# Kernel optimization log

Hardware: AMD Instinct MI355X
Metric: run time of the kernel (lower is better)

Reference implementation:

```python
import jax, jax.numpy as jnp
import numpy as np

H = 8       # n_heads
E = 128     # embedding_size (= per-head dim)
NEG = -1000000000.0


def setup_inputs() -> dict:
    key = jax.random.key(0)
    ks = jax.random.split(key, 12)
    b, n = 8, 1024
    x = jax.random.normal(ks[0], (b, n, E), dtype=jnp.float32)
    dist = jax.random.normal(ks[1], (b, n, n), dtype=jnp.float32)
    mask = jax.random.randint(ks[2], (b, n), 0, 2).astype(jnp.float32)
    s = 1.0 / np.sqrt(E)
    Wq = jax.random.normal(ks[3], (E, H * E), dtype=jnp.float32) * s
    Wk = jax.random.normal(ks[4], (E, H * E), dtype=jnp.float32) * s
    Wv = jax.random.normal(ks[5], (E, H * E), dtype=jnp.float32) * s
    bq = jnp.zeros((H * E,), jnp.float32)
    bk = jnp.zeros((H * E,), jnp.float32)
    bv = jnp.zeros((H * E,), jnp.float32)
    Wo = jax.random.normal(ks[6], (H * E, E), dtype=jnp.float32) * (1.0 / np.sqrt(H * E))
    bo = jnp.zeros((E,), jnp.float32)
    return {"x": x, "dist": dist, "mask": mask, "Wq": Wq, "bq": bq,
            "Wk": Wk, "bk": bk, "Wv": Wv, "bv": bv, "Wo": Wo, "bo": bo}


def reference(x, dist, mask, Wq, bq, Wk, bk, Wv, bv, Wo, bo):
    b, n, e = x.shape
    scale = e ** (-0.5)
    # project and split heads: [b, n, H*E] -> [b, H, n, E]
    def heads(W, bias):
        return (x @ W + bias).reshape(b, n, H, e).transpose(0, 2, 1, 3)
    q = heads(Wq, bq) * mask[:, None, :, None]
    k = heads(Wk, bk) * mask[:, None, :, None]
    v = heads(Wv, bv) * mask[:, None, :, None]
    # scores with additive distance bias broadcast over heads
    a = jnp.einsum('bhqe,bhke->bhqk', q * scale, k) + dist[:, None, :, :]
    am = jnp.einsum('bq,bk->bqk', mask, mask)[:, None, :, :]  # [b,1,n,n]
    a = jnp.where(am == 0, NEG, a)
    a = jax.nn.softmax(a, axis=-1)
    a = jnp.where(am == 0, 0.0, a)
    y = jnp.einsum('bhqk,bhke->bhqe', a, v)
    y = y.transpose(0, 2, 1, 3).reshape(b, n, H * e)
    y = y @ Wo + bo
    return y * mask[:, :, None]
```

## Files before the change

kernel.cpp:

```cpp
#include <hip/hip_runtime.h>
#include <hip/hip_bf16.h>
#include <hip/hip_fp16.h>

#define NH 8
#define ED 128
#define NB 8
#define NN 1024

typedef __attribute__((ext_vector_type(8))) short s16x8;
typedef __attribute__((ext_vector_type(8))) __bf16 bf16x8_t;
typedef __attribute__((ext_vector_type(4))) float f32x4;
typedef __attribute__((ext_vector_type(16))) float f32x16;
typedef __attribute__((ext_vector_type(4))) unsigned int u32x4;

#define LOG2E 1.4426950408889634f
#define SINIT -23.083120654223414f

static __device__ __forceinline__ unsigned short f2bf(float f) {
    union { float f; unsigned u; } v; v.f = f;
    unsigned r = v.u + 0x7fffu + ((v.u >> 16) & 1u);
    return (unsigned short)(r >> 16);
}

static __device__ __forceinline__ f32x4 mfma16(s16x8 a, s16x8 b, f32x4 c) {
    return __builtin_amdgcn_mfma_f32_16x16x32_bf16(
        __builtin_bit_cast(bf16x8_t, a), __builtin_bit_cast(bf16x8_t, b), c, 0, 0, 0);
}

static __device__ __forceinline__ f32x16 mfma32(s16x8 a, s16x8 b, f32x16 c) {
    return __builtin_amdgcn_mfma_f32_32x32x16_bf16(
        __builtin_bit_cast(bf16x8_t, a), __builtin_bit_cast(bf16x8_t, b), c, 0, 0, 0);
}

static __device__ __forceinline__ unsigned cvtpk(float lo, float hi) {
    unsigned r;
    asm("v_cvt_pk_bf16_f32 %0, %1, %2" : "=v"(r) : "v"(lo), "v"(hi));
    return r;
}

static __device__ __forceinline__ void gll16(const void* g, void* l) {
    __builtin_amdgcn_global_load_lds((const __attribute__((address_space(1))) void*)g,
                                     (__attribute__((address_space(3))) void*)l, 16, 0, 0);
}

__global__ __launch_bounds__(256) void prep_xw_kernel(
    const float* __restrict__ x,
    const float* __restrict__ Wq, const float* __restrict__ Wk,
    const float* __restrict__ Wv, const float* __restrict__ Wo,
    unsigned short* __restrict__ xb,
    unsigned short* __restrict__ wqt, unsigned short* __restrict__ wkt,
    unsigned short* __restrict__ wvt, unsigned short* __restrict__ wot) {
    int bid = blockIdx.x, tid = threadIdx.x;
    if (bid < 1024) {
        int i = bid * 256 + tid;
        float4 v = ((const float4*)x)[i];
        unsigned long long pk = (unsigned long long)f2bf(v.x)
                              | ((unsigned long long)f2bf(v.y) << 16)
                              | ((unsigned long long)f2bf(v.z) << 32)
                              | ((unsigned long long)f2bf(v.w) << 48);
        ((unsigned long long*)xb)[i] = pk;
        return;
    }
    __shared__ __align__(16) float wtile[32][36];
    int wi = bid - 1024;
    int mat = wi >> 7, ti = wi & 127;
    const float* in; unsigned short* outp; int rows_in, cols_in, tr0, tc0;
    if (mat == 0)      { in = Wq; outp = wqt; rows_in = 128;  cols_in = 1024; }
    else if (mat == 1) { in = Wk; outp = wkt; rows_in = 128;  cols_in = 1024; }
    else if (mat == 2) { in = Wv; outp = wvt; rows_in = 128;  cols_in = 1024; }
    else               { in = Wo; outp = wot; rows_in = 1024; cols_in = 128;  }
    if (mat < 3) { tr0 = (ti >> 5) * 32; tc0 = (ti & 31) * 32; }
    else         { tr0 = (ti >> 2) * 32; tc0 = (ti & 3)  * 32; }

    {
        int r = tid >> 3, cs = tid & 7;
        f32x4 v = *(const f32x4*)(in + (size_t)(tr0 + r) * cols_in + tc0 + cs * 4);
        *(f32x4*)&wtile[r][cs * 4] = v;
    }
    __syncthreads();
    {
        int c = tid >> 3, rs = tid & 7;
        unsigned long long pk = (unsigned long long)f2bf(wtile[rs * 4 + 0][c])
                              | ((unsigned long long)f2bf(wtile[rs * 4 + 1][c]) << 16)
                              | ((unsigned long long)f2bf(wtile[rs * 4 + 2][c]) << 32)
                              | ((unsigned long long)f2bf(wtile[rs * 4 + 3][c]) << 48);
        *(unsigned long long*)(outp + (size_t)(tc0 + c) * rows_in + tr0 + rs * 4) = pk;
    }
}

__global__ __launch_bounds__(256) void qkv_dist_kernel(
    const unsigned short* __restrict__ xb,
    const unsigned short* __restrict__ wqt,
    const unsigned short* __restrict__ wkt,
    const unsigned short* __restrict__ wvt,
    const float* __restrict__ bq, const float* __restrict__ bk, const float* __restrict__ bv,
    const float* __restrict__ dist,
    const float* __restrict__ mask,
    unsigned short* __restrict__ q_ws,
    unsigned short* __restrict__ k_ws,
    unsigned short* __restrict__ v_ws,
    unsigned short* __restrict__ dswz) {
    int bid = blockIdx.x, tid = threadIdx.x;

    __shared__ __align__(16) unsigned short dt16[128][68];

    if (bid < 1024) {
        int kt = bid & 15;
        int t = bid >> 4;
        int qt = t & 7;
        int b = t >> 3;

        int seg = tid & 15, r0 = tid >> 4;
        const float* src = dist + ((size_t)b * NN + qt * 128) * NN + kt * 64;
        f32x4 m4 = *(const f32x4*)(mask + b * NN + kt * 64 + seg * 4);
#pragma unroll
        for (int pass = 0; pass < 8; ++pass) {
            int row = pass * 16 + r0;
            f32x4 d4 = *(const f32x4*)(src + (size_t)row * NN + seg * 4);
            unsigned long long pk = 0;
#pragma unroll
            for (int j = 0; j < 4; ++j) {
                unsigned short o = (m4[j] == 0.0f) ? (unsigned short)0xFBFF
                                 : __half_as_ushort(__float2half_rn(d4[j] * LOG2E));
                pk |= (unsigned long long)o << (16 * j);
            }
            *(unsigned long long*)&dt16[row][seg * 4] = pk;
        }
        __syncthreads();

        int h = (tid >> 5) & 1;
        int row = (tid >> 6) * 32 + (tid & 31);
#pragma unroll
        for (int c = 0; c < 4; ++c) {
            int colbase = (c >> 1) * 32 + (c & 1) * 16 + 4 * h;
            const unsigned short* rp = &dt16[row][0];
            u32x4 pk;
            pk[0] = *(const unsigned*)&rp[colbase];
            pk[1] = *(const unsigned*)&rp[colbase + 2];
            pk[2] = *(const unsigned*)&rp[colbase + 8];
            pk[3] = *(const unsigned*)&rp[colbase + 10];
            *(u32x4*)(dswz + ((size_t)(bid * 4 + c) * 256 + tid) * 8) = pk;
        }
        return;
    }

    int qb_ = bid - 1024;
    int mt = qb_ / 24, c = qb_ % 24;
    int which = c >> 3;
    int c0 = (c & 7) * 128;
    int m0 = mt * 128;
    int w = tid >> 6, lane = tid & 63, g = lane >> 4, r15 = lane & 15;
    int wr = (w >> 1) * 64, wc = (w & 1) * 64;

    const unsigned short* wt = (which == 0) ? wqt : (which == 1) ? wkt : wvt;
    const float* bias = (which == 0) ? bq : (which == 1) ? bk : bv;

    const f32x4 fzero = {0.f, 0.f, 0.f, 0.f};
    f32x4 acc[4][4];
#pragma unroll
    for (int i = 0; i < 4; i++)
#pragma unroll
        for (int j = 0; j < 4; j++) acc[i][j] = fzero;

#pragma unroll
    for (int kf = 0; kf < 4; kf++) {
        s16x8 af[4], bfr[4];
#pragma unroll
        for (int mf = 0; mf < 4; mf++)
            af[mf] = *(const s16x8*)(xb + (size_t)(m0 + wr + mf * 16 + r15) * ED + kf * 32 + g * 8);
#pragma unroll
        for (int nf = 0; nf < 4; nf++)
            bfr[nf] = *(const s16x8*)(wt + (size_t)(c0 + wc + nf * 16 + r15) * ED + kf * 32 + g * 8);
#pragma unroll
        for (int mf = 0; mf < 4; mf++)
#pragma unroll
            for (int nf = 0; nf < 4; nf++)
                acc[mf][nf] = mfma16(af[mf], bfr[nf], acc[mf][nf]);
    }

    float scale = (which == 0) ? 0.12751741566380696f : 1.0f;

#pragma unroll
    for (int nf = 0; nf < 4; nf++) {
        int col = c0 + wc + nf * 16 + r15;
        float bv_ = bias[col];
        int hh = col >> 7, e = col & 127;
#pragma unroll
        for (int mf = 0; mf < 4; mf++) {
#pragma unroll
            for (int rr = 0; rr < 4; rr++) {
                int row = m0 + wr + mf * 16 + g * 4 + rr;
                int bb = row >> 10, n = row & 1023;
                int bh = bb * NH + hh;
                float val = (acc[mf][nf][rr] + bv_) * scale;
                if (which == 0) {
                    q_ws[((size_t)bh * NN + n) * ED + e] = f2bf(val);
                } else if (which == 1) {
                    int ktl = n >> 6, k = n & 63;
                    int slot = (e >> 4) * 128 + ((e >> 3) & 1) * 64 + (k >> 5) * 32 + (k & 31);
                    k_ws[(size_t)(bh * 16 + ktl) * 8192 + slot * 8 + (e & 7)] = f2bf(val);
                } else {
                    int ktl = n >> 6, k = n & 63;
                    int slot = (k >> 4) * 256 + ((k >> 3) & 1) * 128 + (e >> 5) * 32 + (e & 31);
                    v_ws[(size_t)(bh * 16 + ktl) * 8192 + slot * 8 + (k & 7)] = f2bf(val);
                }
            }
        }
    }
}

__global__ __launch_bounds__(256) void attn_kernel(
    const unsigned short* __restrict__ q_ws,
    const unsigned short* __restrict__ k_ws,
    const unsigned short* __restrict__ v_ws,
    const unsigned short* __restrict__ dswz,
    unsigned short* __restrict__ y_ws) {
    int p = blockIdx.x;
    int b = p & 7, r = p >> 3;
    int head = r >> 3, qt = r & 7;
    int bh = b * NH + head;
    int q0 = qt * 128;

    int tid = threadIdx.x;
    int w = tid >> 6, lane = tid & 63;
    int e31 = lane & 31, h = lane >> 5;

    __shared__ __align__(16) unsigned short Kl[2][8192];
    __shared__ __align__(16) unsigned short Vl[2][8192];

    const char* kg = (const char*)k_ws + (size_t)bh * 16 * 16384;
    const char* vg = (const char*)v_ws + (size_t)bh * 16 * 16384;
    const char* dq = (const char*)dswz + ((size_t)(b * 8 + qt) << 18);

    int qrow = q0 + w * 32 + e31;
    s16x8 qf[8];
    const unsigned short* qb = q_ws + ((size_t)bh * NN + qrow) * ED + h * 8;
#pragma unroll
    for (int es = 0; es < 8; ++es) qf[es] = *(const s16x8*)(qb + es * 16);

    const f32x16 fz16 = {0.f,0.f,0.f,0.f,0.f,0.f,0.f,0.f,0.f,0.f,0.f,0.f,0.f,0.f,0.f,0.f};
    f32x16 sini;
#pragma unroll
    for (int i = 0; i < 16; ++i) sini[i] = SINIT;
    f32x16 o0 = fz16, o1 = fz16, o2 = fz16, o3 = fz16;
    float lacc[4] = {0.f, 0.f, 0.f, 0.f};

#pragma unroll
    for (int pass = 0; pass < 4; ++pass) {
        gll16(kg + (pass * 256 + tid) * 16, (char*)&Kl[0][0] + pass * 4096 + w * 1024);
        gll16(vg + (pass * 256 + tid) * 16, (char*)&Vl[0][0] + pass * 4096 + w * 1024);
    }
    __syncthreads();

    for (int kt = 0; kt < 16; ++kt) {
        int cur = kt & 1;
        if (kt < 15) {
            const char* kn = kg + (size_t)(kt + 1) * 16384;
            const char* vn = vg + (size_t)(kt + 1) * 16384;
            char* kd = (char*)&Kl[cur ^ 1][0] + w * 1024;
            char* vd = (char*)&Vl[cur ^ 1][0] + w * 1024;
#pragma unroll
            for (int pass = 0; pass < 4; ++pass) {
                gll16(kn + (pass * 256 + tid) * 16, kd + pass * 4096);
                gll16(vn + (pass * 256 + tid) * 16, vd + pass * 4096);
            }
        }

        u32x4 dch[4];
#pragma unroll
        for (int c = 0; c < 4; ++c)
            dch[c] = *(const u32x4*)(dq + ((size_t)(kt * 4 + c) * 256 + tid) * 16);

        const char* Kp = (const char*)&Kl[cur][0] + h * 1024 + e31 * 16;
        f32x16 sA0 = sini, sA1 = sini;
        __builtin_amdgcn_s_setprio(1);
#pragma unroll
        for (int es = 0; es < 8; ++es) {
            s16x8 kb0 = *(const s16x8*)(Kp + es * 2048);
            s16x8 kb1 = *(const s16x8*)(Kp + es * 2048 + 512);
            sA0 = mfma32(kb0, qf[es], sA0);
            sA1 = mfma32(kb1, qf[es], sA1);
        }
        __builtin_amdgcn_s_setprio(0);

        float pp[32];
#pragma unroll
        for (int c = 0; c < 4; ++c) {
            float lc = 0.f;
#pragma unroll
            for (int u = 0; u < 8; ++u) {
                int i = c * 8 + u;
                unsigned wv = dch[c][u >> 1];
                float dv = __half2float(__ushort_as_half(
                    (unsigned short)((u & 1) ? (wv >> 16) : (wv & 0xffff))));
                float sv = (i < 16) ? sA0[i] : sA1[i - 16];
                float pv = __builtin_exp2f(sv + dv);
                pp[i] = pv;
                lc += pv;
            }
            lacc[c] += lc;
        }

        const char* Vp = (const char*)&Vl[cur][0] + h * 2048 + e31 * 16;
        __builtin_amdgcn_s_setprio(1);
#pragma unroll
        for (int kf = 0; kf < 2; ++kf) {
#pragma unroll
            for (int ks2 = 0; ks2 < 2; ++ks2) {
                const float* pb = &pp[kf * 16 + ks2 * 8];
                unsigned A0 = cvtpk(pb[0], pb[1]);
                unsigned A1 = cvtpk(pb[2], pb[3]);
                unsigned B0 = cvtpk(pb[4], pb[5]);
                unsigned B1 = cvtpk(pb[6], pb[7]);
                asm("v_permlane32_swap_b32 %0, %1" : "+v"(A0), "+v"(B0));
                asm("v_permlane32_swap_b32 %0, %1" : "+v"(A1), "+v"(B1));
                u32x4 pw;
                pw[0] = A0;
                pw[1] = A1;
                pw[2] = B0;
                pw[3] = B1;
                s16x8 pa = __builtin_bit_cast(s16x8, pw);
                int kstep = kf * 2 + ks2;
                const char* vp = Vp + kstep * 4096;
                o0 = mfma32(pa, *(const s16x8*)(vp), o0);
                o1 = mfma32(pa, *(const s16x8*)(vp + 512), o1);
                o2 = mfma32(pa, *(const s16x8*)(vp + 1024), o2);
                o3 = mfma32(pa, *(const s16x8*)(vp + 1536), o3);
            }
        }
        __builtin_amdgcn_s_setprio(0);
        __syncthreads();
    }

    float l_r = (lacc[0] + lacc[1]) + (lacc[2] + lacc[3]);
    float lt = l_r + __shfl_xor(l_r, 32, 64);
    float inv = (lt > 0.f) ? 1.0f / lt : 0.f;
#pragma unroll
    for (int rc = 0; rc < 4; ++rc) {
#pragma unroll
        for (int jj = 0; jj < 4; ++jj) {
            int qq = jj + 8 * rc + 4 * h;
            float iq = __shfl(inv, qq, 64);
            int row = q0 + w * 32 + qq;
            size_t base = ((size_t)b * NN + row) * (NH * ED) + head * ED + e31;
            y_ws[base]      = f2bf(o0[rc * 4 + jj] * iq);
            y_ws[base + 32] = f2bf(o1[rc * 4 + jj] * iq);
            y_ws[base + 64] = f2bf(o2[rc * 4 + jj] * iq);
            y_ws[base + 96] = f2bf(o3[rc * 4 + jj] * iq);
        }
    }
}

__global__ __launch_bounds__(256) void oproj_kernel(
    const unsigned short* __restrict__ y_ws,
    const unsigned short* __restrict__ wot,
    const float* __restrict__ bo,
    const float* __restrict__ mask,
    float* __restrict__ outp) {
    int bid = blockIdx.x;
    int mt = bid >> 1, nt = bid & 1;
    int m0 = mt * 64, c0 = nt * 64;
    int tid = threadIdx.x;
    int w = tid >> 6, lane = tid & 63, g = lane >> 4, r15 = lane & 15;

    const f32x4 fzero = {0.f, 0.f, 0.f, 0.f};
    f32x4 acc[4];
#pragma unroll
    for (int i = 0; i < 4; i++) acc[i] = fzero;

    const unsigned short* arow = y_ws + (size_t)(m0 + w * 16 + r15) * (NH * ED);
#pragma unroll 4
    for (int kt = 0; kt < 32; ++kt) {
        s16x8 af = *(const s16x8*)(arow + kt * 32 + g * 8);
#pragma unroll
        for (int nf = 0; nf < 4; nf++) {
            s16x8 bfr = *(const s16x8*)(wot + (size_t)(c0 + nf * 16 + r15) * (NH * ED) + kt * 32 + g * 8);
            acc[nf] = mfma16(af, bfr, acc[nf]);
        }
    }
#pragma unroll
    for (int nf = 0; nf < 4; nf++) {
        int col = c0 + nf * 16 + r15;
        float bias = bo[col];
#pragma unroll
        for (int rr = 0; rr < 4; rr++) {
            int token = m0 + w * 16 + g * 4 + rr;
            outp[(size_t)token * ED + col] = (acc[nf][rr] + bias) * mask[token];
        }
    }
}

extern "C" void kernel_launch(void* const* d_in, const int* in_sizes, int n_in,
                              void* d_out, int out_size, void* d_ws, size_t ws_size,
                              hipStream_t stream) {
    const float* x    = (const float*)d_in[0];
    const float* dist = (const float*)d_in[1];
    const float* mask = (const float*)d_in[2];
    const float* Wq   = (const float*)d_in[3];
    const float* bq   = (const float*)d_in[4];
    const float* Wk   = (const float*)d_in[5];
    const float* bk   = (const float*)d_in[6];
    const float* Wv   = (const float*)d_in[7];
    const float* bv   = (const float*)d_in[8];
    const float* Wo   = (const float*)d_in[9];
    const float* bo   = (const float*)d_in[10];
    float* outp = (float*)d_out;

    char* ws = (char*)d_ws;
    unsigned short* xb   = (unsigned short*)(ws);
    unsigned short* wqt  = (unsigned short*)(ws + (2u << 20));
    unsigned short* wkt  = (unsigned short*)(ws + (2u << 20) + (256u << 10));
    unsigned short* wvt  = (unsigned short*)(ws + (2u << 20) + (512u << 10));
    unsigned short* wot  = (unsigned short*)(ws + (2u << 20) + (768u << 10));
    unsigned short* q_ws = (unsigned short*)(ws + (3u << 20));
    unsigned short* k_ws = (unsigned short*)(ws + (19u << 20));
    unsigned short* v_ws = (unsigned short*)(ws + (35u << 20));
    unsigned short* y_ws = (unsigned short*)(ws + (51u << 20));
    unsigned short* dswz = (unsigned short*)(ws + (67u << 20));

    prep_xw_kernel<<<1536, 256, 0, stream>>>(x, Wq, Wk, Wv, Wo, xb, wqt, wkt, wvt, wot);
    qkv_dist_kernel<<<2560, 256, 0, stream>>>(xb, wqt, wkt, wvt, bq, bk, bv,
                                              dist, mask, q_ws, k_ws, v_ws, dswz);
    attn_kernel<<<512, 256, 0, stream>>>(q_ws, k_ws, v_ws, dswz, y_ws);
    oproj_kernel<<<256, 256, 0, stream>>>(y_ws, wot, bo, mask, outp);
}
```

Baseline: 128.2 us.

## Fuse bf16 prep of x and weights into QKV/dist projection kernel

Removes the separate prep kernel. The QKV projection blocks now read fp32 x directly and convert it to bf16 in registers. Each block also loads and transposes its fp32 weight slice into LDS as bf16. The Wo transpose moves into extra blocks of the same launch. This drops one kernel launch and the round trip of x and the weights through the workspace, in exchange for redundant conversion work in each block, higher LDS use, and scalar LDS transpose stores that may bank-conflict.

```diff
diff --git a/kernel.cpp b/kernel.cpp
--- a/kernel.cpp
+++ b/kernel.cpp
@@ -38,73 +38,40 @@
     return r;
 }
 
+static __device__ __forceinline__ s16x8 pack8(const float* p) {
+    f32x4 a = *(const f32x4*)p;
+    f32x4 b = *(const f32x4*)(p + 4);
+    u32x4 u;
+    u[0] = cvtpk(a[0], a[1]);
+    u[1] = cvtpk(a[2], a[3]);
+    u[2] = cvtpk(b[0], b[1]);
+    u[3] = cvtpk(b[2], b[3]);
+    return __builtin_bit_cast(s16x8, u);
+}
+
 static __device__ __forceinline__ void gll16(const void* g, void* l) {
     __builtin_amdgcn_global_load_lds((const __attribute__((address_space(1))) void*)g,
                                      (__attribute__((address_space(3))) void*)l, 16, 0, 0);
 }
 
-__global__ __launch_bounds__(256) void prep_xw_kernel(
+__global__ __launch_bounds__(256) void fused_kernel(
     const float* __restrict__ x,
     const float* __restrict__ Wq, const float* __restrict__ Wk,
     const float* __restrict__ Wv, const float* __restrict__ Wo,
-    unsigned short* __restrict__ xb,
-    unsigned short* __restrict__ wqt, unsigned short* __restrict__ wkt,
-    unsigned short* __restrict__ wvt, unsigned short* __restrict__ wot) {
-    int bid = blockIdx.x, tid = threadIdx.x;
-    if (bid < 1024) {
-        int i = bid * 256 + tid;
-        float4 v = ((const float4*)x)[i];
-        unsigned long long pk = (unsigned long long)f2bf(v.x)
-                              | ((unsigned long long)f2bf(v.y) << 16)
-                              | ((unsigned long long)f2bf(v.z) << 32)
-                              | ((unsigned long long)f2bf(v.w) << 48);
-        ((unsigned long long*)xb)[i] = pk;
-        return;
-    }
-    __shared__ __align__(16) float wtile[32][36];
-    int wi = bid - 1024;
-    int mat = wi >> 7, ti = wi & 127;
-    const float* in; unsigned short* outp; int rows_in, cols_in, tr0, tc0;
-    if (mat == 0)      { in = Wq; outp = wqt; rows_in = 128;  cols_in = 1024; }
-    else if (mat == 1) { in = Wk; outp = wkt; rows_in = 128;  cols_in = 1024; }
-    else if (mat == 2) { in = Wv; outp = wvt; rows_in = 128;  cols_in = 1024; }
-    else               { in = Wo; outp = wot; rows_in = 1024; cols_in = 128;  }
-    if (mat < 3) { tr0 = (ti >> 5) * 32; tc0 = (ti & 31) * 32; }
-    else         { tr0 = (ti >> 2) * 32; tc0 = (ti & 3)  * 32; }
-
-    {
-        int r = tid >> 3, cs = tid & 7;
-        f32x4 v = *(const f32x4*)(in + (size_t)(tr0 + r) * cols_in + tc0 + cs * 4);
-        *(f32x4*)&wtile[r][cs * 4] = v;
-    }
-    __syncthreads();
-    {
-        int c = tid >> 3, rs = tid & 7;
-        unsigned long long pk = (unsigned long long)f2bf(wtile[rs * 4 + 0][c])
-                              | ((unsigned long long)f2bf(wtile[rs * 4 + 1][c]) << 16)
-                              | ((unsigned long long)f2bf(wtile[rs * 4 + 2][c]) << 32)
-                              | ((unsigned long long)f2bf(wtile[rs * 4 + 3][c]) << 48);
-        *(unsigned long long*)(outp + (size_t)(tc0 + c) * rows_in + tr0 + rs * 4) = pk;
-    }
-}
-
-__global__ __launch_bounds__(256) void qkv_dist_kernel(
-    const unsigned short* __restrict__ xb,
-    const unsigned short* __restrict__ wqt,
-    const unsigned short* __restrict__ wkt,
-    const unsigned short* __restrict__ wvt,
     const float* __restrict__ bq, const float* __restrict__ bk, const float* __restrict__ bv,
     const float* __restrict__ dist,
     const float* __restrict__ mask,
     unsigned short* __restrict__ q_ws,
     unsigned short* __restrict__ k_ws,
     unsigned short* __restrict__ v_ws,
-    unsigned short* __restrict__ dswz) {
+    unsigned short* __restrict__ dswz,
+    unsigned short* __restrict__ wot) {
     int bid = blockIdx.x, tid = threadIdx.x;
 
-    __shared__ __align__(16) unsigned short dt16[128][68];
+    __shared__ __align__(16) char smem[34816];
 
     if (bid < 1024) {
+        unsigned short (*dt16)[68] = (unsigned short (*)[68])smem;
         int kt = bid & 15;
         int t = bid >> 4;
         int qt = t & 7;
@@ -144,7 +111,29 @@
         return;
     }
 
-    int qb_ = bid - 1024;
+    if (bid < 1152) {
+        float (*wtile)[36] = (float (*)[36])smem;
+        int ti = bid - 1024;
+        int tr0 = (ti >> 2) * 32, tc0 = (ti & 3) * 32;
+        {
+            int r = tid >> 3, cs = tid & 7;
+            f32x4 v = *(const f32x4*)(Wo + (size_t)(tr0 + r) * 128 + tc0 + cs * 4);
+            *(f32x4*)&wtile[r][cs * 4] = v;
+        }
+        __syncthreads();
+        {
+            int c = tid >> 3, rs = tid & 7;
+            unsigned long long pk = (unsigned long long)f2bf(wtile[rs * 4 + 0][c])
+                                  | ((unsigned long long)f2bf(wtile[rs * 4 + 1][c]) << 16)
+                                  | ((unsigned long long)f2bf(wtile[rs * 4 + 2][c]) << 32)
+                                  | ((unsigned long long)f2bf(wtile[rs * 4 + 3][c]) << 48);
+            *(unsigned long long*)(wot + (size_t)(tc0 + c) * 1024 + tr0 + rs * 4) = pk;
+        }
+        return;
+    }
+
+    unsigned short (*wlds)[136] = (unsigned short (*)[136])smem;
+    int qb_ = bid - 1152;
     int mt = qb_ / 24, c = qb_ % 24;
     int which = c >> 3;
     int c0 = (c & 7) * 128;
@@ -152,8 +141,19 @@
     int w = tid >> 6, lane = tid & 63, g = lane >> 4, r15 = lane & 15;
     int wr = (w >> 1) * 64, wc = (w & 1) * 64;
 
-    const unsigned short* wt = (which == 0) ? wqt : (which == 1) ? wkt : wvt;
+    const float* Wsrc = (which == 0) ? Wq : (which == 1) ? Wk : Wv;
     const float* bias = (which == 0) ? bq : (which == 1) ? bk : bv;
+
+#pragma unroll
+    for (int pass = 0; pass < 16; ++pass) {
+        int idx = pass * 256 + tid;
+        int e = idx >> 5, cs = idx & 31;
+        f32x4 v = *(const f32x4*)(Wsrc + (size_t)e * 1024 + c0 + cs * 4);
+#pragma unroll
+        for (int j = 0; j < 4; ++j)
+            wlds[cs * 4 + j][e] = f2bf(v[j]);
+    }
+    __syncthreads();
 
     const f32x4 fzero = {0.f, 0.f, 0.f, 0.f};
     f32x4 acc[4][4];
@@ -167,10 +167,10 @@
         s16x8 af[4], bfr[4];
 #pragma unroll
         for (int mf = 0; mf < 4; mf++)
-            af[mf] = *(const s16x8*)(xb + (size_t)(m0 + wr + mf * 16 + r15) * ED + kf * 32 + g * 8);
+            af[mf] = pack8(x + (size_t)(m0 + wr + mf * 16 + r15) * ED + kf * 32 + g * 8);
 #pragma unroll
         for (int nf = 0; nf < 4; nf++)
-            bfr[nf] = *(const s16x8*)(wt + (size_t)(c0 + wc + nf * 16 + r15) * ED + kf * 32 + g * 8);
+            bfr[nf] = *(const s16x8*)&wlds[wc + nf * 16 + r15][kf * 32 + g * 8];
 #pragma unroll
         for (int mf = 0; mf < 4; mf++)
 #pragma unroll
@@ -407,10 +407,6 @@
     float* outp = (float*)d_out;
 
     char* ws = (char*)d_ws;
-    unsigned short* xb   = (unsigned short*)(ws);
-    unsigned short* wqt  = (unsigned short*)(ws + (2u << 20));
-    unsigned short* wkt  = (unsigned short*)(ws + (2u << 20) + (256u << 10));
-    unsigned short* wvt  = (unsigned short*)(ws + (2u << 20) + (512u << 10));
     unsigned short* wot  = (unsigned short*)(ws + (2u << 20) + (768u << 10));
     unsigned short* q_ws = (unsigned short*)(ws + (3u << 20));
     unsigned short* k_ws = (unsigned short*)(ws + (19u << 20));
@@ -418,9 +414,8 @@
     unsigned short* y_ws = (unsigned short*)(ws + (51u << 20));
     unsigned short* dswz = (unsigned short*)(ws + (67u << 20));
 
-    prep_xw_kernel<<<1536, 256, 0, stream>>>(x, Wq, Wk, Wv, Wo, xb, wqt, wkt, wvt, wot);
-    qkv_dist_kernel<<<2560, 256, 0, stream>>>(xb, wqt, wkt, wvt, bq, bk, bv,
-                                              dist, mask, q_ws, k_ws, v_ws, dswz);
+    fused_kernel<<<2688, 256, 0, stream>>>(x, Wq, Wk, Wv, Wo, bq, bk, bv,
+                                           dist, mask, q_ws, k_ws, v_ws, dswz, wot);
     attn_kernel<<<512, 256, 0, stream>>>(q_ws, k_ws, v_ws, dswz, y_ws);
     oproj_kernel<<<256, 256, 0, stream>>>(y_ws, wot, bo, mask, outp);
 }
```

Measured after the change: 130.3 us. No clear change (+1.6%).
